# Kernel optimization log

Hardware: AMD Instinct MI355X
Metric: run time of the kernel (lower is better)

## Reference

```python
import jax, jax.numpy as jnp
import numpy as np

TEMPERATURE = 0.05
REDUCTION = "mean"
EPS = 1e-12

B, LQ, LK, D = 128, 256, 512, 1024


def l2_normalize(x):
    # torch F.normalize: x / clamp(||x||_2, min=eps)
    n = jnp.sqrt(jnp.sum(x * x, axis=-1, keepdims=True))
    return x / jnp.maximum(n, EPS)


def setup_inputs() -> dict:
    key = jax.random.key(0)
    k1, k2, k3, k4, k5, k6 = jax.random.split(key, 6)
    return {
        "query": jax.random.normal(k1, (B, LQ, D), dtype=jnp.float32),
        "pos_key": jax.random.normal(k2, (B, LK, D), dtype=jnp.float32),
        "neg_key": jax.random.normal(k3, (B, LK, D), dtype=jnp.float32),
        "query_mask": jax.random.randint(k4, (B, LQ), 0, 2, dtype=jnp.int32),
        "pos_mask": jax.random.randint(k5, (B, LK), 0, 2, dtype=jnp.int32),
        "neg_mask": jax.random.randint(k6, (B, LK), 0, 2, dtype=jnp.int32),
    }


def _maxsim_logit(q, k, k_mask, q_mask):
    # q: [B, Lq, D] (normalized), k: [B, Lk, D] (normalized)
    sim = jnp.einsum("bqd,bkd->bqk", q, k)  # [B, Lq, Lk]
    sim = sim * k_mask[:, None, :].astype(sim.dtype)  # mask keys (multiplicative, as in source)
    m = jnp.max(sim, axis=-1)  # [B, Lq]
    return jnp.sum(m * q_mask.astype(m.dtype), axis=-1, keepdims=True)  # [B, 1]


def reference(query, pos_key, neg_key, query_mask, pos_mask, neg_mask):
    q = l2_normalize(query)
    pk = l2_normalize(pos_key)
    nk = l2_normalize(neg_key)
    pos_logit = _maxsim_logit(q, pk, pos_mask, query_mask)  # [B, 1]
    neg_logit = _maxsim_logit(q, nk, neg_mask, query_mask)  # [B, 1]
    logits = jnp.concatenate([pos_logit, neg_logit], axis=1) / TEMPERATURE  # [B, 2]
    # cross-entropy with target class 0
    logp = jax.nn.log_softmax(logits, axis=-1)
    nll = -logp[:, 0]  # [B]
    if REDUCTION == "mean":
        return jnp.mean(nll)
    elif REDUCTION == "sum":
        return jnp.sum(nll)
    return nll
```

## Files before the change

### kernel.cpp

```cpp
#include <hip/hip_runtime.h>
#include <hip/hip_fp16.h>
#include <math.h>


constexpr int NB = 128;
constexpr int LQ = 256;
constexpr int LK = 512;
constexpr int DD = 1024;

#define TEMP_INV 20.0f
#define EPSN 1e-12f

typedef __fp16 fp16x2 __attribute__((ext_vector_type(2)));
typedef _Float16 f16x8 __attribute__((ext_vector_type(8)));
typedef float f32x4 __attribute__((ext_vector_type(4)));

#define BM 128
#define BN 128
#define BK 32
#define KITERS (DD / BK)

__device__ inline f16x8 cvt8(float4 a, float4 b) {
  union { f16x8 v; fp16x2 h[4]; } u;
  u.h[0] = __builtin_amdgcn_cvt_pkrtz(a.x, a.y);
  u.h[1] = __builtin_amdgcn_cvt_pkrtz(a.z, a.w);
  u.h[2] = __builtin_amdgcn_cvt_pkrtz(b.x, b.y);
  u.h[3] = __builtin_amdgcn_cvt_pkrtz(b.z, b.w);
  return u.v;
}

__device__ __forceinline__ int lidx(int row, int ch) {
  const int line = row >> 1;
  const int slot = ((ch | ((row & 1) << 2)) ^ (line & 7));
  return line * 64 + slot * 8;
}

__global__ __launch_bounds__(512, 4) void maxsim_kernel(
    const float* __restrict__ q, const float* __restrict__ pk,
    const float* __restrict__ nk, const int* __restrict__ pmask,
    const int* __restrict__ nmask, float* __restrict__ part) {
  __shared__ _Float16 __align__(16) As[2][BM * BK];
  __shared__ _Float16 __align__(16) Bs[2][BN * BK];

  const int bid = blockIdx.x;
  const int sw = (bid & 7) * 256 + (bid >> 3);
  const int b = sw >> 4;
  const int x = sw & 15;
  const int mt = x >> 3;
  const int nt = (x >> 1) & 3;
  const int kt = x & 1;

  const float* kbase = kt ? nk : pk;
  const int* mbase = kt ? nmask : pmask;

  const float* Ag = q + ((size_t)b * LQ + mt * BM) * DD;
  const float* Bg = kbase + ((size_t)b * LK + nt * BN) * DD;

  const int tid = threadIdx.x;
  const int lane = tid & 63;
  const int w = tid >> 6;
  const int wr = w >> 1;
  const int wc = w & 1;
  const int frow = lane & 15;
  const int kgrp = lane >> 4;

  const int rowS = tid >> 2;
  const int chS = tid & 3;
  const float* pA = Ag + (size_t)rowS * DD + chS * 8;
  const float* pB = Bg + (size_t)rowS * DD + chS * 8;
  const int sidx = lidx(rowS, chS);

  float ssqA = 0.f, ssqB = 0.f;
  f32x4 acc[2][4] = {};

  auto LOADS = [&](int it, float4& a0, float4& a1, float4& b0, float4& b1) {
    const int koff = it * BK;
    a0 = *(const float4*)(pA + koff);
    a1 = *(const float4*)(pA + koff + 4);
    b0 = *(const float4*)(pB + koff);
    b1 = *(const float4*)(pB + koff + 4);
  };
  auto STORE = [&](int bsel, float4 a0, float4 a1, float4 b0, float4 b1) {
    ssqA += a0.x * a0.x + a0.y * a0.y + a0.z * a0.z + a0.w * a0.w +
            a1.x * a1.x + a1.y * a1.y + a1.z * a1.z + a1.w * a1.w;
    ssqB += b0.x * b0.x + b0.y * b0.y + b0.z * b0.z + b0.w * b0.w +
            b1.x * b1.x + b1.y * b1.y + b1.z * b1.z + b1.w * b1.w;
    *(f16x8*)&As[bsel][sidx] = cvt8(a0, a1);
    *(f16x8*)&Bs[bsel][sidx] = cvt8(b0, b1);
  };
  auto COMPUTE = [&](int bsel) {
    __builtin_amdgcn_s_setprio(1);
    f16x8 af[2], bf[4];
    #pragma unroll
    for (int m = 0; m < 2; ++m)
      af[m] = *(const f16x8*)&As[bsel][lidx(wr * 32 + m * 16 + frow, kgrp)];
    #pragma unroll
    for (int n = 0; n < 4; ++n)
      bf[n] = *(const f16x8*)&Bs[bsel][lidx(wc * 64 + n * 16 + frow, kgrp)];
    #pragma unroll
    for (int m = 0; m < 2; ++m)
      #pragma unroll
      for (int n = 0; n < 4; ++n)
        acc[m][n] = __builtin_amdgcn_mfma_f32_16x16x32_f16(af[m], bf[n], acc[m][n], 0, 0, 0);
    __builtin_amdgcn_s_setprio(0);
  };

  {
    float4 a0, a1, b0, b1;
    LOADS(0, a0, a1, b0, b1);
    STORE(0, a0, a1, b0, b1);
  }
  __syncthreads();

  #pragma unroll
  for (int it = 0; it < KITERS - 1; ++it) {
    float4 a0, a1, b0, b1;
    LOADS(it + 1, a0, a1, b0, b1);
    __builtin_amdgcn_sched_barrier(0);
    COMPUTE(it & 1);
    STORE((it & 1) ^ 1, a0, a1, b0, b1);
    __syncthreads();
  }
  COMPUTE(1);

  ssqA += __shfl_xor(ssqA, 1); ssqA += __shfl_xor(ssqA, 2);
  ssqB += __shfl_xor(ssqB, 1); ssqB += __shfl_xor(ssqB, 2);

  float* const aux = reinterpret_cast<float*>(&As[0][0]);
  float* const csc = aux;
  float* const invA_s = aux + BN;
  float* const rmax = aux + BN + BM;

  if (chS == 0) {
    invA_s[rowS] = 1.0f / fmaxf(sqrtf(ssqA), EPSN);
    const int key = nt * BN + rowS;
    csc[rowS] = (mbase[(size_t)b * LK + key] ? 1.0f : 0.0f) /
                fmaxf(sqrtf(ssqB), EPSN);
  }
  __syncthreads();

  float vmax[2][4];
  #pragma unroll
  for (int m = 0; m < 2; ++m)
    #pragma unroll
    for (int r = 0; r < 4; ++r) vmax[m][r] = -INFINITY;
  #pragma unroll
  for (int n = 0; n < 4; ++n) {
    const float s = csc[wc * 64 + n * 16 + frow];
    #pragma unroll
    for (int m = 0; m < 2; ++m)
      #pragma unroll
      for (int r = 0; r < 4; ++r)
        vmax[m][r] = fmaxf(vmax[m][r], acc[m][n][r] * s);
  }
  #pragma unroll
  for (int off = 1; off < 16; off <<= 1)
    #pragma unroll
    for (int m = 0; m < 2; ++m)
      #pragma unroll
      for (int r = 0; r < 4; ++r)
        vmax[m][r] = fmaxf(vmax[m][r], __shfl_xor(vmax[m][r], off));
  if ((lane & 15) == 0) {
    #pragma unroll
    for (int m = 0; m < 2; ++m)
      #pragma unroll
      for (int r = 0; r < 4; ++r)
        rmax[(wr * 32 + m * 16 + kgrp * 4 + r) * 2 + wc] = vmax[m][r];
  }
  __syncthreads();
  if (tid < BM) {
    const float v = fmaxf(rmax[tid * 2], rmax[tid * 2 + 1]) * invA_s[tid];
    part[(((size_t)kt * NB + b) * 4 + nt) * LQ + mt * BM + tid] = v;
  }
}

__global__ __launch_bounds__(256) void logits_kernel(
    const float* __restrict__ part, const int* __restrict__ qmask,
    float* __restrict__ nll) {
  int b = blockIdx.x;
  int t = threadIdx.x;
  float mp = -INFINITY, mn = -INFINITY;
  #pragma unroll
  for (int ntile = 0; ntile < 4; ++ntile) {
    mp = fmaxf(mp, part[(((size_t)0 * NB + b) * 4 + ntile) * LQ + t]);
    mn = fmaxf(mn, part[(((size_t)1 * NB + b) * 4 + ntile) * LQ + t]);
  }
  float qm = qmask[(size_t)b * LQ + t] ? 1.0f : 0.0f;
  float p = mp * qm;
  float n = mn * qm;
  #pragma unroll
  for (int o = 32; o; o >>= 1) { p += __shfl_down(p, o); n += __shfl_down(n, o); }
  __shared__ float sp[4], sn[4];
  int lane = t & 63, w = t >> 6;
  if (lane == 0) { sp[w] = p; sn[w] = n; }
  __syncthreads();
  if (t == 0) {
    float ps = sp[0] + sp[1] + sp[2] + sp[3];
    float ns = sn[0] + sn[1] + sn[2] + sn[3];
    float z = (ns - ps) * TEMP_INV;
    nll[b] = z > 0.0f ? z + log1pf(expf(-z)) : log1pf(expf(z));
  }
}

__global__ void finalize_kernel(const float* __restrict__ nll, float* __restrict__ out) {
  __shared__ float s[128];
  int t = threadIdx.x;
  s[t] = nll[t];
  __syncthreads();
  #pragma unroll
  for (int o = 64; o; o >>= 1) {
    if (t < o) s[t] += s[t + o];
    __syncthreads();
  }
  if (t == 0) out[0] = s[0] * (1.0f / 128.0f);
}

extern "C" void kernel_launch(void* const* d_in, const int* in_sizes, int n_in,
                              void* d_out, int out_size, void* d_ws, size_t ws_size,
                              hipStream_t stream) {
  const float* q = (const float*)d_in[0];
  const float* pk = (const float*)d_in[1];
  const float* nk = (const float*)d_in[2];
  const int* qm = (const int*)d_in[3];
  const int* pm = (const int*)d_in[4];
  const int* nm = (const int*)d_in[5];

  float* ws = (float*)d_ws;
  float* part = ws;
  float* nll = part + 262144;

  maxsim_kernel<<<2048, 512, 0, stream>>>(q, pk, nk, pm, nm, part);
  logits_kernel<<<NB, 256, 0, stream>>>(part, qm, nll);
  finalize_kernel<<<1, 128, 0, stream>>>(nll, (float*)d_out);
}
```

Before: 180.9 us.

## Fuse positive and negative key GEMMs per block to reuse query tiles

Each block now handles both the positive and negative key tiles for the same query tile. The query fragment is loaded and converted once and reused for two sets of MFMAs, so the grid is halved. This removes redundant global reads and fp16 conversion of the query, which was previously done twice. The cost is higher register pressure from doubled accumulators and more LDS, which may lower occupancy under the 512x4 launch bounds.

```diff
diff --git a/kernel.cpp b/kernel.cpp
--- a/kernel.cpp
+++ b/kernel.cpp
@@ -18,7 +18,7 @@
 #define BM 128
 #define BN 128
 #define BK 32
-#define KITERS (DD / BK)
+#define KITERS 32
 
 __device__ inline f16x8 cvt8(float4 a, float4 b) {
   union { f16x8 v; fp16x2 h[4]; } u;
@@ -29,9 +29,9 @@
   return u.v;
 }
 
-__device__ __forceinline__ int lidx(int row, int ch) {
+__device__ __forceinline__ int lidxR(int row, int kg) {
   const int line = row >> 1;
-  const int slot = ((ch | ((row & 1) << 2)) ^ (line & 7));
+  const int slot = (kg | ((row & 1) << 2)) ^ (line & 7);
   return line * 64 + slot * 8;
 }
 
@@ -40,21 +40,19 @@
     const float* __restrict__ nk, const int* __restrict__ pmask,
     const int* __restrict__ nmask, float* __restrict__ part) {
   __shared__ _Float16 __align__(16) As[2][BM * BK];
-  __shared__ _Float16 __align__(16) Bs[2][BN * BK];
+  __shared__ _Float16 __align__(16) Bps[2][BN * BK];
+  __shared__ _Float16 __align__(16) Bns[2][BN * BK];
 
   const int bid = blockIdx.x;
-  const int sw = (bid & 7) * 256 + (bid >> 3);
-  const int b = sw >> 4;
-  const int x = sw & 15;
-  const int mt = x >> 3;
-  const int nt = (x >> 1) & 3;
-  const int kt = x & 1;
-
-  const float* kbase = kt ? nk : pk;
-  const int* mbase = kt ? nmask : pmask;
+  const int sw = (bid & 7) * 128 + (bid >> 3);
+  const int b = sw >> 3;
+  const int x = sw & 7;
+  const int mt = x >> 2;
+  const int nt = x & 3;
 
   const float* Ag = q + ((size_t)b * LQ + mt * BM) * DD;
-  const float* Bg = kbase + ((size_t)b * LK + nt * BN) * DD;
+  const float* Pg = pk + ((size_t)b * LK + nt * BN) * DD;
+  const float* Ng = nk + ((size_t)b * LK + nt * BN) * DD;
 
   const int tid = threadIdx.x;
   const int lane = tid & 63;
@@ -67,110 +65,139 @@
   const int rowS = tid >> 2;
   const int chS = tid & 3;
   const float* pA = Ag + (size_t)rowS * DD + chS * 8;
-  const float* pB = Bg + (size_t)rowS * DD + chS * 8;
-  const int sidx = lidx(rowS, chS);
-
-  float ssqA = 0.f, ssqB = 0.f;
-  f32x4 acc[2][4] = {};
-
-  auto LOADS = [&](int it, float4& a0, float4& a1, float4& b0, float4& b1) {
+  const float* pP = Pg + (size_t)rowS * DD + chS * 8;
+  const float* pN = Ng + (size_t)rowS * DD + chS * 8;
+  const int sidx = lidxR(rowS, chS);
+
+  float ssqA = 0.f, ssqP = 0.f, ssqN = 0.f;
+  f32x4 accp[2][4] = {};
+  f32x4 accn[2][4] = {};
+
+  auto LOADS = [&](int it, float4& a0, float4& a1, float4& p0, float4& p1,
+                   float4& n0, float4& n1) {
     const int koff = it * BK;
     a0 = *(const float4*)(pA + koff);
     a1 = *(const float4*)(pA + koff + 4);
-    b0 = *(const float4*)(pB + koff);
-    b1 = *(const float4*)(pB + koff + 4);
+    p0 = *(const float4*)(pP + koff);
+    p1 = *(const float4*)(pP + koff + 4);
+    n0 = *(const float4*)(pN + koff);
+    n1 = *(const float4*)(pN + koff + 4);
   };
-  auto STORE = [&](int bsel, float4 a0, float4 a1, float4 b0, float4 b1) {
+  auto STORE = [&](int bsel, float4 a0, float4 a1, float4 p0, float4 p1,
+                   float4 n0, float4 n1) {
     ssqA += a0.x * a0.x + a0.y * a0.y + a0.z * a0.z + a0.w * a0.w +
             a1.x * a1.x + a1.y * a1.y + a1.z * a1.z + a1.w * a1.w;
-    ssqB += b0.x * b0.x + b0.y * b0.y + b0.z * b0.z + b0.w * b0.w +
-            b1.x * b1.x + b1.y * b1.y + b1.z * b1.z + b1.w * b1.w;
+    ssqP += p0.x * p0.x + p0.y * p0.y + p0.z * p0.z + p0.w * p0.w +
+            p1.x * p1.x + p1.y * p1.y + p1.z * p1.z + p1.w * p1.w;
+    ssqN += n0.x * n0.x + n0.y * n0.y + n0.z * n0.z + n0.w * n0.w +
+            n1.x * n1.x + n1.y * n1.y + n1.z * n1.z + n1.w * n1.w;
     *(f16x8*)&As[bsel][sidx] = cvt8(a0, a1);
-    *(f16x8*)&Bs[bsel][sidx] = cvt8(b0, b1);
+    *(f16x8*)&Bps[bsel][sidx] = cvt8(p0, p1);
+    *(f16x8*)&Bns[bsel][sidx] = cvt8(n0, n1);
   };
   auto COMPUTE = [&](int bsel) {
     __builtin_amdgcn_s_setprio(1);
-    f16x8 af[2], bf[4];
-    #pragma unroll
-    for (int m = 0; m < 2; ++m)
-      af[m] = *(const f16x8*)&As[bsel][lidx(wr * 32 + m * 16 + frow, kgrp)];
-    #pragma unroll
-    for (int n = 0; n < 4; ++n)
-      bf[n] = *(const f16x8*)&Bs[bsel][lidx(wc * 64 + n * 16 + frow, kgrp)];
-    #pragma unroll
-    for (int m = 0; m < 2; ++m)
-      #pragma unroll
-      for (int n = 0; n < 4; ++n)
-        acc[m][n] = __builtin_amdgcn_mfma_f32_16x16x32_f16(af[m], bf[n], acc[m][n], 0, 0, 0);
+    f16x8 af[2];
+    #pragma unroll
+    for (int m = 0; m < 2; ++m)
+      af[m] = *(const f16x8*)&As[bsel][lidxR(wr * 32 + m * 16 + frow, kgrp)];
+    #pragma unroll
+    for (int n = 0; n < 4; ++n) {
+      const int ro = lidxR(wc * 64 + n * 16 + frow, kgrp);
+      f16x8 bp = *(const f16x8*)&Bps[bsel][ro];
+      f16x8 bn = *(const f16x8*)&Bns[bsel][ro];
+      #pragma unroll
+      for (int m = 0; m < 2; ++m) {
+        accp[m][n] = __builtin_amdgcn_mfma_f32_16x16x32_f16(af[m], bp, accp[m][n], 0, 0, 0);
+        accn[m][n] = __builtin_amdgcn_mfma_f32_16x16x32_f16(af[m], bn, accn[m][n], 0, 0, 0);
+      }
+    }
     __builtin_amdgcn_s_setprio(0);
   };
 
   {
-    float4 a0, a1, b0, b1;
-    LOADS(0, a0, a1, b0, b1);
-    STORE(0, a0, a1, b0, b1);
+    float4 a0, a1, p0, p1, n0, n1;
+    LOADS(0, a0, a1, p0, p1, n0, n1);
+    STORE(0, a0, a1, p0, p1, n0, n1);
   }
   __syncthreads();
 
   #pragma unroll
   for (int it = 0; it < KITERS - 1; ++it) {
-    float4 a0, a1, b0, b1;
-    LOADS(it + 1, a0, a1, b0, b1);
+    float4 a0, a1, p0, p1, n0, n1;
+    LOADS(it + 1, a0, a1, p0, p1, n0, n1);
     __builtin_amdgcn_sched_barrier(0);
     COMPUTE(it & 1);
-    STORE((it & 1) ^ 1, a0, a1, b0, b1);
+    STORE((it & 1) ^ 1, a0, a1, p0, p1, n0, n1);
     __syncthreads();
   }
   COMPUTE(1);
 
   ssqA += __shfl_xor(ssqA, 1); ssqA += __shfl_xor(ssqA, 2);
-  ssqB += __shfl_xor(ssqB, 1); ssqB += __shfl_xor(ssqB, 2);
+  ssqP += __shfl_xor(ssqP, 1); ssqP += __shfl_xor(ssqP, 2);
+  ssqN += __shfl_xor(ssqN, 1); ssqN += __shfl_xor(ssqN, 2);
 
   float* const aux = reinterpret_cast<float*>(&As[0][0]);
-  float* const csc = aux;
-  float* const invA_s = aux + BN;
-  float* const rmax = aux + BN + BM;
+  float* const invA_s = aux;
+  float* const cscP = aux + 128;
+  float* const cscN = aux + 256;
+  float* const rmaxP = aux + 384;
+  float* const rmaxN = aux + 640;
 
   if (chS == 0) {
     invA_s[rowS] = 1.0f / fmaxf(sqrtf(ssqA), EPSN);
     const int key = nt * BN + rowS;
-    csc[rowS] = (mbase[(size_t)b * LK + key] ? 1.0f : 0.0f) /
-                fmaxf(sqrtf(ssqB), EPSN);
-  }
-  __syncthreads();
-
-  float vmax[2][4];
+    cscP[rowS] = (pmask[(size_t)b * LK + key] ? 1.0f : 0.0f) /
+                 fmaxf(sqrtf(ssqP), EPSN);
+    cscN[rowS] = (nmask[(size_t)b * LK + key] ? 1.0f : 0.0f) /
+                 fmaxf(sqrtf(ssqN), EPSN);
+  }
+  __syncthreads();
+
+  float vmp[2][4], vmn[2][4];
   #pragma unroll
   for (int m = 0; m < 2; ++m)
     #pragma unroll
-    for (int r = 0; r < 4; ++r) vmax[m][r] = -INFINITY;
+    for (int r = 0; r < 4; ++r) { vmp[m][r] = -INFINITY; vmn[m][r] = -INFINITY; }
   #pragma unroll
   for (int n = 0; n < 4; ++n) {
-    const float s = csc[wc * 64 + n * 16 + frow];
-    #pragma unroll
-    for (int m = 0; m < 2; ++m)
-      #pragma unroll
-      for (int r = 0; r < 4; ++r)
-        vmax[m][r] = fmaxf(vmax[m][r], acc[m][n][r] * s);
+    const int col = wc * 64 + n * 16 + frow;
+    const float sp = cscP[col];
+    const float sn = cscN[col];
+    #pragma unroll
+    for (int m = 0; m < 2; ++m)
+      #pragma unroll
+      for (int r = 0; r < 4; ++r) {
+        vmp[m][r] = fmaxf(vmp[m][r], accp[m][n][r] * sp);
+        vmn[m][r] = fmaxf(vmn[m][r], accn[m][n][r] * sn);
+      }
   }
   #pragma unroll
   for (int off = 1; off < 16; off <<= 1)
     #pragma unroll
     for (int m = 0; m < 2; ++m)
       #pragma unroll
-      for (int r = 0; r < 4; ++r)
-        vmax[m][r] = fmaxf(vmax[m][r], __shfl_xor(vmax[m][r], off));
+      for (int r = 0; r < 4; ++r) {
+        vmp[m][r] = fmaxf(vmp[m][r], __shfl_xor(vmp[m][r], off));
+        vmn[m][r] = fmaxf(vmn[m][r], __shfl_xor(vmn[m][r], off));
+      }
   if ((lane & 15) == 0) {
     #pragma unroll
     for (int m = 0; m < 2; ++m)
       #pragma unroll
-      for (int r = 0; r < 4; ++r)
-        rmax[(wr * 32 + m * 16 + kgrp * 4 + r) * 2 + wc] = vmax[m][r];
+      for (int r = 0; r < 4; ++r) {
+        const int row = wr * 32 + m * 16 + kgrp * 4 + r;
+        rmaxP[row * 2 + wc] = vmp[m][r];
+        rmaxN[row * 2 + wc] = vmn[m][r];
+      }
   }
   __syncthreads();
   if (tid < BM) {
-    const float v = fmaxf(rmax[tid * 2], rmax[tid * 2 + 1]) * invA_s[tid];
-    part[(((size_t)kt * NB + b) * 4 + nt) * LQ + mt * BM + tid] = v;
+    const float ia = invA_s[tid];
+    const float vP = fmaxf(rmaxP[tid * 2], rmaxP[tid * 2 + 1]) * ia;
+    const float vN = fmaxf(rmaxN[tid * 2], rmaxN[tid * 2 + 1]) * ia;
+    part[(((size_t)0 * NB + b) * 4 + nt) * LQ + mt * BM + tid] = vP;
+    part[(((size_t)1 * NB + b) * 4 + nt) * LQ + mt * BM + tid] = vN;
   }
 }
 
@@ -229,7 +256,7 @@
   float* part = ws;
   float* nll = part + 262144;
 
-  maxsim_kernel<<<2048, 512, 0, stream>>>(q, pk, nk, pm, nm, part);
+  maxsim_kernel<<<1024, 512, 0, stream>>>(q, pk, nk, pm, nm, part);
   logits_kernel<<<NB, 256, 0, stream>>>(part, qm, nll);
   finalize_kernel<<<1, 128, 0, stream>>>(nll, (float*)d_out);
 }
```

Result: slower. 186.3 us (+2.9%).
